# Kernel optimization log

Hardware: AMD Instinct MI355X
Metric: run time of the kernel (lower is better)

The kernel has to match this reference:

```python
import jax, jax.numpy as jnp
import numpy as np
from jax import lax

D_MODEL = 256
D_STATE = 16
BATCH = 4
SEQ = 16384
LN_EPS = 1e-5


def setup_inputs() -> dict:
    key = jax.random.key(0)
    ks = jax.random.split(key, 16)
    d, s = D_MODEL, D_STATE
    lim = 1.0 / np.sqrt(d)
    u = lambda k, shape, l: jax.random.uniform(k, shape, jnp.float32, -l, l)
    return {
        "x": jax.random.normal(ks[0], (BATCH, SEQ, d), jnp.float32),
        # forward branch params (torch Linear stored as (in, out))
        "W_fproj": u(ks[1], (d, 2 * d), lim),
        "b_fproj": u(ks[2], (2 * d,), lim),
        "A_f": jax.random.normal(ks[3], (s, d), jnp.float32),
        "W_fgate": u(ks[4], (d, s), lim),
        "b_fgate": u(ks[5], (s,), lim),
        # backward branch params
        "W_bproj": u(ks[6], (d, 2 * d), lim),
        "b_bproj": u(ks[7], (2 * d,), lim),
        "A_b": jax.random.normal(ks[8], (s, d), jnp.float32),
        "W_bgate": u(ks[9], (d, s), lim),
        "b_bgate": u(ks[10], (s,), lim),
        # output proj + layernorm
        "W_out": u(ks[11], (2 * d, d), 1.0 / np.sqrt(2 * d)),
        "b_out": u(ks[12], (d,), 1.0 / np.sqrt(2 * d)),
        "ln_g": jnp.ones((d,), jnp.float32),
        "ln_b": jnp.zeros((d,), jnp.float32),
    }


def _scan_dir(x, W_proj, b_proj, A, W_gate, b_gate):
    """One direction: gated state-space scan. x: (B,S,D) -> (B,S,D)."""
    B, S, D = x.shape
    proj = x @ W_proj + b_proj            # (B,S,2D)
    value = proj[..., D:]                 # the 'gate' chunk is unused in the original
    gw = jax.nn.sigmoid(value @ W_gate + b_gate)  # (B,S,d_state)

    def step(state, inp):
        g, v = inp                        # g:(B,Ns), v:(B,D)
        gi = g[:, :, None]                # (B,Ns,1)
        upd = A[None, :, :] * v[:, None, :]
        state = state * gi + upd * (1.0 - gi)
        out = (state * gi).sum(axis=1)    # (B,D)
        return state, out

    init = jnp.zeros((B, A.shape[0], D), x.dtype)
    _, outs = lax.scan(step, init, (gw.transpose(1, 0, 2), value.transpose(1, 0, 2)))
    return outs.transpose(1, 0, 2)        # (B,S,D)


def reference(x, W_fproj, b_fproj, A_f, W_fgate, b_fgate,
              W_bproj, b_bproj, A_b, W_bgate, b_bgate,
              W_out, b_out, ln_g, ln_b):
    fwd = _scan_dir(x, W_fproj, b_fproj, A_f, W_fgate, b_fgate)
    x_rev = jnp.flip(x, axis=1)
    bwd = jnp.flip(_scan_dir(x_rev, W_bproj, b_bproj, A_b, W_bgate, b_bgate), axis=1)
    combined = jnp.concatenate([fwd, bwd], axis=-1)    # (B,S,2D)
    out = combined @ W_out + b_out                     # (B,S,D)
    mu = out.mean(axis=-1, keepdims=True)
    var = out.var(axis=-1, keepdims=True)
    out = (out - mu) * lax.rsqrt(var + LN_EPS) * ln_g + ln_b
    return out  # dropout is identity in eval mode
```

## Files before the change

### kernel.cpp

```cpp
#include <hip/hip_runtime.h>

#define SEQ   16384
#define NB    4
#define NROWS 65536
#define NC    512
#define CL    32

typedef short bf16x8 __attribute__((ext_vector_type(8)));
typedef float f32x4  __attribute__((ext_vector_type(4)));
typedef float f32x2  __attribute__((ext_vector_type(2)));

__device__ inline float bf2f(ushort u) {
    unsigned int t = ((unsigned int)u) << 16;
    float f; __builtin_memcpy(&f, &t, 4); return f;
}
__device__ inline ushort f2bf(float f) {
    unsigned int b; __builtin_memcpy(&b, &f, 4);
    unsigned int r = (b + 0x7FFFu + ((b >> 16) & 1u)) >> 16;
    return (ushort)r;
}

__global__ __launch_bounds__(256) void prep_weights(
    const float* __restrict__ Wf, const float* __restrict__ Wb,
    const float* __restrict__ Wo, const float* __restrict__ Wgf,
    const float* __restrict__ Wgb, const float* __restrict__ bfp,
    const float* __restrict__ bbp,
    ushort* __restrict__ BTv, ushort* __restrict__ WoT,
    ushort* __restrict__ WgT, float* __restrict__ bias_v)
{
    int idx = blockIdx.x * 256 + threadIdx.x;
    if (idx < 131072) {
        int dir = idx >> 16, j = idx & 65535, n = j >> 8, k = j & 255;
        const float* W = dir ? Wb : Wf;
        BTv[idx] = f2bf(W[k * 512 + 256 + n]);
    } else if (idx < 262144) {
        int j = idx - 131072; int n = j >> 9, k = j & 511;
        WoT[j] = f2bf(Wo[k * 256 + n]);
    } else if (idx < 270336) {
        int j = idx - 262144; int dir = j >> 12, jj = j & 4095, s = jj >> 8, k = jj & 255;
        WgT[j] = f2bf((dir ? Wgb : Wgf)[k * 16 + s]);
    } else if (idx < 270848) {
        int j = idx - 270336; int dir = j >> 8, n = j & 255;
        bias_v[j] = (dir ? bbp : bfp)[256 + n];
    }
}

__global__ __launch_bounds__(512) void gemm_value(
    const float* __restrict__ x, const ushort* __restrict__ BTv,
    const float* __restrict__ bias_v, ushort* __restrict__ value)
{
    __shared__ ushort Al[128 * 40];
    __shared__ ushort Bl[256 * 40];
    const int tid = threadIdx.x;
    const int m0 = blockIdx.x * 128, dir = blockIdx.y;
    const ushort* BT = BTv + dir * 65536;
    const int w = tid >> 6, l = tid & 63;
    const int wr = w >> 2, wc = w & 3;
    const int l15 = l & 15, lk = (l >> 4) * 8;
    f32x4 acc[4][4] = {};

    for (int kk = 0; kk < 256; kk += 32) {
        {
            int r = tid >> 2, c = (tid & 3) * 8;
            const float* xp = x + (size_t)(m0 + r) * 256 + kk + c;
            float4 a = *(const float4*)xp;
            float4 b = *(const float4*)(xp + 4);
            ushort u[8];
            u[0] = f2bf(a.x); u[1] = f2bf(a.y); u[2] = f2bf(a.z); u[3] = f2bf(a.w);
            u[4] = f2bf(b.x); u[5] = f2bf(b.y); u[6] = f2bf(b.z); u[7] = f2bf(b.w);
            *(uint4*)&Al[r * 40 + c] = *(uint4*)u;
        }
        #pragma unroll
        for (int i = 0; i < 2; ++i) {
            int idx = tid + i * 512; int r = idx >> 2, c = idx & 3;
            *(uint4*)&Bl[r * 40 + c * 8] = *(const uint4*)(BT + (size_t)r * 256 + kk + c * 8);
        }
        __syncthreads();
        bf16x8 af[4], bfr[4];
        #pragma unroll
        for (int m = 0; m < 4; ++m) af[m] = *(const bf16x8*)&Al[(wr * 64 + m * 16 + l15) * 40 + lk];
        #pragma unroll
        for (int n = 0; n < 4; ++n) bfr[n] = *(const bf16x8*)&Bl[(wc * 64 + n * 16 + l15) * 40 + lk];
        #pragma unroll
        for (int m = 0; m < 4; ++m)
            #pragma unroll
            for (int n = 0; n < 4; ++n)
                acc[m][n] = __builtin_amdgcn_mfma_f32_16x16x32_bf16(af[m], bfr[n], acc[m][n], 0, 0, 0);
        __syncthreads();
    }
    const int rbase = (l >> 4) * 4;
    #pragma unroll
    for (int m = 0; m < 4; ++m)
        #pragma unroll
        for (int n = 0; n < 4; ++n) {
            int col = wc * 64 + n * 16 + l15;
            float bv = bias_v[dir * 256 + col];
            #pragma unroll
            for (int r = 0; r < 4; ++r) {
                int row = m0 + wr * 64 + m * 16 + rbase + r;
                value[(size_t)row * 512 + dir * 256 + col] = f2bf(acc[m][n][r] + bv);
            }
        }
}

__global__ __launch_bounds__(256) void gate_mfma(
    const ushort* __restrict__ value, const ushort* __restrict__ WgT,
    const float* __restrict__ bgf, const float* __restrict__ bgb,
    float* __restrict__ gw)
{
    __shared__ ushort Av[64 * 264];
    const int tid = threadIdx.x;
    const int r0 = blockIdx.x * 64, dir = blockIdx.y;
    #pragma unroll
    for (int i = 0; i < 8; ++i) {
        int idx = tid + i * 256; int r = idx >> 5, c = idx & 31;
        *(uint4*)&Av[r * 264 + c * 8] =
            *(const uint4*)(value + (size_t)(r0 + r) * 512 + dir * 256 + c * 8);
    }
    __syncthreads();
    const int w = tid >> 6, l = tid & 63, l15 = l & 15, lk = (l >> 4) * 8;
    const ushort* Wg = WgT + dir * 4096;
    f32x4 acc = {};
    #pragma unroll
    for (int kk = 0; kk < 256; kk += 32) {
        bf16x8 af = *(const bf16x8*)&Av[(w * 16 + l15) * 264 + kk + lk];
        bf16x8 bf = *(const bf16x8*)(Wg + l15 * 256 + kk + lk);
        acc = __builtin_amdgcn_mfma_f32_16x16x32_bf16(af, bf, acc, 0, 0, 0);
    }
    const float* bg = dir ? bgb : bgf;
    float bgs = bg[l15];
    const int rbase = (l >> 4) * 4;
    #pragma unroll
    for (int r = 0; r < 4; ++r) {
        int gr = r0 + w * 16 + rbase + r;
        int b = gr >> 14, t = gr & 16383;
        float sv = 1.f / (1.f + __expf(-(acc[r] + bgs)));
        gw[((size_t)(dir * NB + b) * SEQ + t) * 16 + l15] = sv;
    }
}

__global__ __launch_bounds__(128) void pass_a(
    const ushort* __restrict__ value, const float* __restrict__ gw,
    float* __restrict__ L, float* __restrict__ P)
{
    const int chunk = blockIdx.x, b = blockIdx.y, dir = blockIdx.z;
    const int tid = threadIdx.x;
    __shared__ float gs[CL * 16];
    const float* gwd = gw + ((size_t)(dir * NB + b) * SEQ + chunk * CL) * 16;
    ((float4*)gs)[tid] = ((const float4*)gwd)[tid];
    __syncthreads();
    const ushort* vb = value + ((size_t)b * SEQ + chunk * CL) * 512 + dir * 256 + tid * 2;
    f32x2 c[16] = {};
    for (int i = 0; i < CL; ++i) {
        int row = dir ? (CL - 1 - i) : i;
        uint vv = *(const uint*)(vb + (size_t)row * 512);
        f32x2 v; v.x = bf2f((ushort)(vv & 0xffffu)); v.y = bf2f((ushort)(vv >> 16));
        float g[16];
        #pragma unroll
        for (int q = 0; q < 4; ++q)
            *(float4*)&g[q * 4] = *(const float4*)&gs[row * 16 + q * 4];
        #pragma unroll
        for (int s = 0; s < 16; ++s) {
            f32x2 gg; gg.x = g[s]; gg.y = g[s];
            c[s] = v + gg * (c[s] - v);
        }
    }
    float* Lp = L + ((size_t)(dir * NB + b) * NC + chunk) * 4096 + tid * 2;
    #pragma unroll
    for (int s = 0; s < 16; ++s)
        *(f32x2*)(Lp + s * 256) = c[s];
    if (tid < 16) {
        float p = 1.f;
        for (int t = 0; t < CL; ++t) p *= gs[t * 16 + tid];
        P[((size_t)(dir * NB + b) * NC + chunk) * 16 + tid] = p;
    }
}

__global__ __launch_bounds__(128) void chunk_scan(
    float* __restrict__ L, const float* __restrict__ P)
{
    const int bid = blockIdx.x;
    const int dir = bid >> 7, b = (bid >> 5) & 3, s = (bid >> 1) & 15, dh = bid & 1;
    const int d = dh * 128 + threadIdx.x;
    const size_t cb = (size_t)(dir * NB + b) * NC;
    float* Lb = L + cb * 4096 + s * 256 + d;
    const float* Pb = P + cb * 16 + s;
    float e = 0.f;
    float lA[16], pA[16], lB[16], pB[16];

#define LOADB(la, pa, ib) { _Pragma("unroll") \
    for (int j = 0; j < 16; ++j) { \
        int t = (ib) * 16 + j; int k = dir ? (NC - 1 - t) : t; \
        la[j] = Lb[(size_t)k * 4096]; pa[j] = Pb[k * 16]; } }
#define PROCB(la, pa, ib) { _Pragma("unroll") \
    for (int j = 0; j < 16; ++j) { \
        int t = (ib) * 16 + j; int k = dir ? (NC - 1 - t) : t; \
        Lb[(size_t)k * 4096] = e; e = pa[j] * e + la[j]; } }

    LOADB(lA, pA, 0)
    for (int ib = 0; ib < 32; ib += 2) {
        LOADB(lB, pB, ib + 1)
        PROCB(lA, pA, ib)
        if (ib + 2 < 32) { LOADB(lA, pA, ib + 2) }
        PROCB(lB, pB, ib + 1)
    }
#undef LOADB
#undef PROCB
}

__global__ __launch_bounds__(128) void pass_c(
    ushort* __restrict__ value, const float* __restrict__ gw,
    const float* __restrict__ L, const float* __restrict__ A_f,
    const float* __restrict__ A_b)
{
    const int chunk = blockIdx.x, b = blockIdx.y, dir = blockIdx.z;
    const int tid = threadIdx.x;
    __shared__ float gs[CL * 16];
    const float* gwd = gw + ((size_t)(dir * NB + b) * SEQ + chunk * CL) * 16;
    ((float4*)gs)[tid] = ((const float4*)gwd)[tid];
    __syncthreads();
    ushort* vb = value + ((size_t)b * SEQ + chunk * CL) * 512 + dir * 256 + tid * 2;
    const float* Ad = dir ? A_b : A_f;
    const float* Lp = L + ((size_t)(dir * NB + b) * NC + chunk) * 4096 + tid * 2;
    f32x2 a[16], c[16];
    #pragma unroll
    for (int s = 0; s < 16; ++s) {
        a[s] = *(const f32x2*)(Ad + s * 256 + tid * 2);
        c[s] = *(const f32x2*)(Lp + s * 256);
    }
    for (int i = 0; i < CL; ++i) {
        int row = dir ? (CL - 1 - i) : i;
        uint vv = *(const uint*)(vb + (size_t)row * 512);
        f32x2 v; v.x = bf2f((ushort)(vv & 0xffffu)); v.y = bf2f((ushort)(vv >> 16));
        float g[16];
        #pragma unroll
        for (int q = 0; q < 4; ++q)
            *(float4*)&g[q * 4] = *(const float4*)&gs[row * 16 + q * 4];
        f32x2 o = {0.f, 0.f};
        #pragma unroll
        for (int s = 0; s < 16; ++s) {
            f32x2 gg; gg.x = g[s]; gg.y = g[s];
            c[s] = v + gg * (c[s] - v);
            o += a[s] * (gg * c[s]);
        }
        uint outv = (uint)f2bf(o.x) | ((uint)f2bf(o.y) << 16);
        *(uint*)(vb + (size_t)row * 512) = outv;
    }
}

__global__ __launch_bounds__(512) void gemm_out_ln(
    const ushort* __restrict__ A, const ushort* __restrict__ BT,
    const float* __restrict__ b_out, const float* __restrict__ ln_g,
    const float* __restrict__ ln_b, float* __restrict__ out)
{
    __shared__ ushort Al[128 * 40];
    __shared__ ushort Bl[256 * 40];
    __shared__ float red[2][2][4][64];
    const int tid = threadIdx.x;
    const int m0 = blockIdx.x * 128;
    const int w = tid >> 6, l = tid & 63;
    const int wr = w >> 2, wc = w & 3;
    const int l15 = l & 15, lk = (l >> 4) * 8;
    f32x4 acc[4][4] = {};

    for (int kk = 0; kk < 512; kk += 32) {
        {
            int r = tid >> 2, c = tid & 3;
            *(uint4*)&Al[r * 40 + c * 8] = *(const uint4*)(A + (size_t)(m0 + r) * 512 + kk + c * 8);
        }
        #pragma unroll
        for (int i = 0; i < 2; ++i) {
            int idx = tid + i * 512; int r = idx >> 2, c = idx & 3;
            *(uint4*)&Bl[r * 40 + c * 8] = *(const uint4*)(BT + (size_t)r * 512 + kk + c * 8);
        }
        __syncthreads();
        bf16x8 af[4], bfr[4];
        #pragma unroll
        for (int m = 0; m < 4; ++m) af[m] = *(const bf16x8*)&Al[(wr * 64 + m * 16 + l15) * 40 + lk];
        #pragma unroll
        for (int n = 0; n < 4; ++n) bfr[n] = *(const bf16x8*)&Bl[(wc * 64 + n * 16 + l15) * 40 + lk];
        #pragma unroll
        for (int m = 0; m < 4; ++m)
            #pragma unroll
            for (int n = 0; n < 4; ++n)
                acc[m][n] = __builtin_amdgcn_mfma_f32_16x16x32_bf16(af[m], bfr[n], acc[m][n], 0, 0, 0);
        __syncthreads();
    }
    const int rbase = (l >> 4) * 4;
    float gg[4], bb[4];
    #pragma unroll
    for (int n = 0; n < 4; ++n) {
        int col = wc * 64 + n * 16 + l15;
        float bv = b_out[col];
        gg[n] = ln_g[col]; bb[n] = ln_b[col];
        #pragma unroll
        for (int m = 0; m < 4; ++m)
            #pragma unroll
            for (int r = 0; r < 4; ++r)
                acc[m][n][r] += bv;
    }
    float s1[4][4], s2[4][4];
    #pragma unroll
    for (int m = 0; m < 4; ++m)
        #pragma unroll
        for (int r = 0; r < 4; ++r) {
            float a_ = 0.f, b_ = 0.f;
            #pragma unroll
            for (int n = 0; n < 4; ++n) {
                float v = acc[m][n][r];
                a_ += v; b_ += v * v;
            }
            s1[m][r] = a_; s2[m][r] = b_;
        }
    #pragma unroll
    for (int mask = 1; mask < 16; mask <<= 1)
        #pragma unroll
        for (int m = 0; m < 4; ++m)
            #pragma unroll
            for (int r = 0; r < 4; ++r) {
                s1[m][r] += __shfl_xor(s1[m][r], mask, 64);
                s2[m][r] += __shfl_xor(s2[m][r], mask, 64);
            }
    if (l15 == 0) {
        #pragma unroll
        for (int m = 0; m < 4; ++m)
            #pragma unroll
            for (int r = 0; r < 4; ++r) {
                int row = m * 16 + rbase + r;
                red[0][wr][wc][row] = s1[m][r];
                red[1][wr][wc][row] = s2[m][r];
            }
    }
    __syncthreads();
    #pragma unroll
    for (int m = 0; m < 4; ++m)
        #pragma unroll
        for (int r = 0; r < 4; ++r) {
            int row = m * 16 + rbase + r;
            float t1 = red[0][wr][0][row] + red[0][wr][1][row] + red[0][wr][2][row] + red[0][wr][3][row];
            float t2 = red[1][wr][0][row] + red[1][wr][1][row] + red[1][wr][2][row] + red[1][wr][3][row];
            float mu = t1 * (1.f / 256.f);
            float var = t2 * (1.f / 256.f) - mu * mu;
            float rs = rsqrtf(var + 1e-5f);
            #pragma unroll
            for (int n = 0; n < 4; ++n) {
                int col = wc * 64 + n * 16 + l15;
                out[(size_t)(m0 + wr * 64 + row) * 256 + col] = (acc[m][n][r] - mu) * rs * gg[n] + bb[n];
            }
        }
}

extern "C" void kernel_launch(void* const* d_in, const int* in_sizes, int n_in,
                              void* d_out, int out_size, void* d_ws, size_t ws_size,
                              hipStream_t stream)
{
    const float* x       = (const float*)d_in[0];
    const float* W_fproj = (const float*)d_in[1];
    const float* b_fproj = (const float*)d_in[2];
    const float* A_f     = (const float*)d_in[3];
    const float* W_fgate = (const float*)d_in[4];
    const float* b_fgate = (const float*)d_in[5];
    const float* W_bproj = (const float*)d_in[6];
    const float* b_bproj = (const float*)d_in[7];
    const float* A_b     = (const float*)d_in[8];
    const float* W_bgate = (const float*)d_in[9];
    const float* b_bgate = (const float*)d_in[10];
    const float* W_out   = (const float*)d_in[11];
    const float* b_out   = (const float*)d_in[12];
    const float* ln_g    = (const float*)d_in[13];
    const float* ln_b    = (const float*)d_in[14];

    char* ws = (char*)d_ws;
    ushort* value  = (ushort*)(ws + 0);
    float*  gw     = (float*) (ws + 67108864);
    float*  L      = (float*) (ws + 75497472);
    float*  P      = (float*) (ws + 142606336);
    ushort* BTv    = (ushort*)(ws + 142868480);
    ushort* WoT    = (ushort*)(ws + 143130624);
    ushort* WgT    = (ushort*)(ws + 143392768);
    float*  bias_v = (float*) (ws + 143409152);

    prep_weights<<<1058, 256, 0, stream>>>(W_fproj, W_bproj, W_out, W_fgate, W_bgate,
                                           b_fproj, b_bproj, BTv, WoT, WgT, bias_v);
    gemm_value<<<dim3(512, 2), 512, 0, stream>>>(x, BTv, bias_v, value);
    gate_mfma<<<dim3(1024, 2), 256, 0, stream>>>(value, WgT, b_fgate, b_bgate, gw);
    pass_a<<<dim3(NC, NB, 2), 128, 0, stream>>>(value, gw, L, P);
    chunk_scan<<<256, 128, 0, stream>>>(L, P);
    pass_c<<<dim3(NC, NB, 2), 128, 0, stream>>>(value, gw, L, A_f, A_b);
    gemm_out_ln<<<512, 512, 0, stream>>>(value, WoT, b_out, ln_g, ln_b, (float*)d_out);
}
```

Baseline: 223.5 us.

## Fuse gate projection with chunk-local scan pass and prefetch values in pass_c

Merges the gate MFMA kernel with the first chunk-scan pass. The value tile already in shared memory and the freshly computed gates are reused to produce per-chunk local states and gate products, so the separate pass_a launch and its global re-reads of value and gw go away. pass_c now software-prefetches value rows four at a time to hide load latency, and occupancy hints are added to several kernels' launch bounds. The fused kernel does more serial work per block and uses more shared memory, which may lower occupancy.

```diff
diff --git a/kernel.cpp b/kernel.cpp
--- a/kernel.cpp
+++ b/kernel.cpp
@@ -103,12 +103,13 @@
         }
 }
 
-__global__ __launch_bounds__(256) void gate_mfma(
+__global__ __launch_bounds__(256, 3) void gate_scan(
     const ushort* __restrict__ value, const ushort* __restrict__ WgT,
     const float* __restrict__ bgf, const float* __restrict__ bgb,
-    float* __restrict__ gw)
+    float* __restrict__ gw, float* __restrict__ L, float* __restrict__ P)
 {
     __shared__ ushort Av[64 * 264];
+    __shared__ float gsm[64 * 16];
     const int tid = threadIdx.x;
     const int r0 = blockIdx.x * 64, dir = blockIdx.y;
     #pragma unroll
@@ -127,56 +128,46 @@
         bf16x8 bf = *(const bf16x8*)(Wg + l15 * 256 + kk + lk);
         acc = __builtin_amdgcn_mfma_f32_16x16x32_bf16(af, bf, acc, 0, 0, 0);
     }
-    const float* bg = dir ? bgb : bgf;
-    float bgs = bg[l15];
+    const float bgs = (dir ? bgb : bgf)[l15];
     const int rbase = (l >> 4) * 4;
+    const int b = r0 >> 14, t0 = r0 & 16383;
     #pragma unroll
     for (int r = 0; r < 4; ++r) {
-        int gr = r0 + w * 16 + rbase + r;
-        int b = gr >> 14, t = gr & 16383;
+        int lr = w * 16 + rbase + r;
         float sv = 1.f / (1.f + __expf(-(acc[r] + bgs)));
-        gw[((size_t)(dir * NB + b) * SEQ + t) * 16 + l15] = sv;
-    }
-}
-
-__global__ __launch_bounds__(128) void pass_a(
-    const ushort* __restrict__ value, const float* __restrict__ gw,
-    float* __restrict__ L, float* __restrict__ P)
-{
-    const int chunk = blockIdx.x, b = blockIdx.y, dir = blockIdx.z;
-    const int tid = threadIdx.x;
-    __shared__ float gs[CL * 16];
-    const float* gwd = gw + ((size_t)(dir * NB + b) * SEQ + chunk * CL) * 16;
-    ((float4*)gs)[tid] = ((const float4*)gwd)[tid];
+        gsm[lr * 16 + l15] = sv;
+        gw[((size_t)(dir * NB + b) * SEQ + t0 + lr) * 16 + l15] = sv;
+    }
     __syncthreads();
-    const ushort* vb = value + ((size_t)b * SEQ + chunk * CL) * 512 + dir * 256 + tid * 2;
+    const int ci = tid >> 7, dp = tid & 127;
+    const int chunk = (t0 >> 5) + ci;
     f32x2 c[16] = {};
     for (int i = 0; i < CL; ++i) {
         int row = dir ? (CL - 1 - i) : i;
-        uint vv = *(const uint*)(vb + (size_t)row * 512);
+        uint vv = *(const uint*)&Av[(ci * 32 + row) * 264 + dp * 2];
         f32x2 v; v.x = bf2f((ushort)(vv & 0xffffu)); v.y = bf2f((ushort)(vv >> 16));
         float g[16];
         #pragma unroll
         for (int q = 0; q < 4; ++q)
-            *(float4*)&g[q * 4] = *(const float4*)&gs[row * 16 + q * 4];
+            *(float4*)&g[q * 4] = *(const float4*)&gsm[(ci * 32 + row) * 16 + q * 4];
         #pragma unroll
         for (int s = 0; s < 16; ++s) {
             f32x2 gg; gg.x = g[s]; gg.y = g[s];
             c[s] = v + gg * (c[s] - v);
         }
     }
-    float* Lp = L + ((size_t)(dir * NB + b) * NC + chunk) * 4096 + tid * 2;
+    float* Lp = L + ((size_t)(dir * NB + b) * NC + chunk) * 4096 + dp * 2;
     #pragma unroll
     for (int s = 0; s < 16; ++s)
         *(f32x2*)(Lp + s * 256) = c[s];
-    if (tid < 16) {
+    if (dp < 16) {
         float p = 1.f;
-        for (int t = 0; t < CL; ++t) p *= gs[t * 16 + tid];
-        P[((size_t)(dir * NB + b) * NC + chunk) * 16 + tid] = p;
-    }
-}
-
-__global__ __launch_bounds__(128) void chunk_scan(
+        for (int t = 0; t < CL; ++t) p *= gsm[(ci * 32 + t) * 16 + dp];
+        P[((size_t)(dir * NB + b) * NC + chunk) * 16 + dp] = p;
+    }
+}
+
+__global__ __launch_bounds__(128, 2) void chunk_scan(
     float* __restrict__ L, const float* __restrict__ P)
 {
     const int bid = blockIdx.x;
@@ -208,7 +199,7 @@
 #undef PROCB
 }
 
-__global__ __launch_bounds__(128) void pass_c(
+__global__ __launch_bounds__(128, 3) void pass_c(
     ushort* __restrict__ value, const float* __restrict__ gw,
     const float* __restrict__ L, const float* __restrict__ A_f,
     const float* __restrict__ A_b)
@@ -228,23 +219,43 @@
         a[s] = *(const f32x2*)(Ad + s * 256 + tid * 2);
         c[s] = *(const f32x2*)(Lp + s * 256);
     }
-    for (int i = 0; i < CL; ++i) {
-        int row = dir ? (CL - 1 - i) : i;
-        uint vv = *(const uint*)(vb + (size_t)row * 512);
-        f32x2 v; v.x = bf2f((ushort)(vv & 0xffffu)); v.y = bf2f((ushort)(vv >> 16));
-        float g[16];
-        #pragma unroll
-        for (int q = 0; q < 4; ++q)
-            *(float4*)&g[q * 4] = *(const float4*)&gs[row * 16 + q * 4];
-        f32x2 o = {0.f, 0.f};
-        #pragma unroll
-        for (int s = 0; s < 16; ++s) {
-            f32x2 gg; gg.x = g[s]; gg.y = g[s];
-            c[s] = v + gg * (c[s] - v);
-            o += a[s] * (gg * c[s]);
-        }
-        uint outv = (uint)f2bf(o.x) | ((uint)f2bf(o.y) << 16);
-        *(uint*)(vb + (size_t)row * 512) = outv;
+    uint vbuf[4];
+    #pragma unroll
+    for (int j = 0; j < 4; ++j) {
+        int row = dir ? (CL - 1 - j) : j;
+        vbuf[j] = *(const uint*)(vb + (size_t)row * 512);
+    }
+    for (int i0 = 0; i0 < CL; i0 += 4) {
+        uint vcur[4];
+        #pragma unroll
+        for (int j = 0; j < 4; ++j) vcur[j] = vbuf[j];
+        if (i0 + 4 < CL) {
+            #pragma unroll
+            for (int j = 0; j < 4; ++j) {
+                int t = i0 + 4 + j;
+                int row = dir ? (CL - 1 - t) : t;
+                vbuf[j] = *(const uint*)(vb + (size_t)row * 512);
+            }
+        }
+        #pragma unroll
+        for (int j = 0; j < 4; ++j) {
+            int t = i0 + j;
+            int row = dir ? (CL - 1 - t) : t;
+            f32x2 v; v.x = bf2f((ushort)(vcur[j] & 0xffffu)); v.y = bf2f((ushort)(vcur[j] >> 16));
+            float g[16];
+            #pragma unroll
+            for (int q = 0; q < 4; ++q)
+                *(float4*)&g[q * 4] = *(const float4*)&gs[row * 16 + q * 4];
+            f32x2 o = {0.f, 0.f};
+            #pragma unroll
+            for (int s = 0; s < 16; ++s) {
+                f32x2 gg; gg.x = g[s]; gg.y = g[s];
+                c[s] = v + gg * (c[s] - v);
+                o += a[s] * (gg * c[s]);
+            }
+            uint outv = (uint)f2bf(o.x) | ((uint)f2bf(o.y) << 16);
+            *(uint*)(vb + (size_t)row * 512) = outv;
+        }
     }
 }
 
@@ -383,8 +394,7 @@
     prep_weights<<<1058, 256, 0, stream>>>(W_fproj, W_bproj, W_out, W_fgate, W_bgate,
                                            b_fproj, b_bproj, BTv, WoT, WgT, bias_v);
     gemm_value<<<dim3(512, 2), 512, 0, stream>>>(x, BTv, bias_v, value);
-    gate_mfma<<<dim3(1024, 2), 256, 0, stream>>>(value, WgT, b_fgate, b_bgate, gw);
-    pass_a<<<dim3(NC, NB, 2), 128, 0, stream>>>(value, gw, L, P);
+    gate_scan<<<dim3(1024, 2), 256, 0, stream>>>(value, WgT, b_fgate, b_bgate, gw, L, P);
     chunk_scan<<<256, 128, 0, stream>>>(L, P);
     pass_c<<<dim3(NC, NB, 2), 128, 0, stream>>>(value, gw, L, A_f, A_b);
     gemm_out_ln<<<512, 512, 0, stream>>>(value, WoT, b_out, ln_g, ln_b, (float*)d_out);
```

After: 207.3 us. 7.3% less time.
